# Performance work log

Hardware: AMD Instinct MI355X
Metric: run time of the kernel (lower is better)

The kernel has to match this reference:

```python
import jax, jax.numpy as jnp
import numpy as np

B, T, S, D, V, NX = 4, 256, 400, 512, 50000, 50
VEXT = V + NX  # extended vocab


def setup_inputs() -> dict:
    key = jax.random.key(0)
    ks = jax.random.split(key, 10)
    s = 0.02
    return {
        "x": jax.random.normal(ks[0], (B, T, D), dtype=jnp.float32),
        "enc_outputs": jax.random.normal(ks[1], (B, S, D), dtype=jnp.float32),
        "src_mask": jax.random.randint(ks[2], (B, 1, S), 0, 2, dtype=jnp.int32),
        "enc_batch_extend_vocab": jax.random.randint(ks[3], (B, S), 0, VEXT, dtype=jnp.int64),
        "extra_zeros": jnp.zeros((B, T, NX), dtype=jnp.float32),
        "fc_w": jax.random.normal(ks[4], (V, D), dtype=jnp.float32) * s,
        "fc_b": jnp.zeros((V,), dtype=jnp.float32),
        "pgen_w": jax.random.normal(ks[5], (1, D), dtype=jnp.float32) * s,
        "pgen_b": jnp.zeros((1,), dtype=jnp.float32),
        "wq": jax.random.normal(ks[6], (D, D), dtype=jnp.float32) * s,
        "bq": jnp.zeros((D,), dtype=jnp.float32),
        "wk": jax.random.normal(ks[7], (D, D), dtype=jnp.float32) * s,
        "bk": jnp.zeros((D,), dtype=jnp.float32),
    }


def reference(x, enc_outputs, src_mask, enc_batch_extend_vocab, extra_zeros,
              fc_w, fc_b, pgen_w, pgen_b, wq, bq, wk, bk):
    # vocab distribution: [B,T,V]
    p_vocab = jax.nn.softmax(x @ fc_w.T + fc_b, axis=-1)
    # single-head cross attention probs (h=1 -> d_k = D)
    q = x @ wq.T + bq                 # [B,T,D]
    k = enc_outputs @ wk.T + bk       # [B,S,D]
    scores = jnp.einsum('btd,bsd->bts', q, k) / jnp.sqrt(jnp.float32(D))
    scores = jnp.where(src_mask == 0, jnp.float32(-1e9), scores)  # mask [B,1,S]
    attn_probs = jax.nn.softmax(scores, axis=-1)  # [B,T,S]
    # generation gate
    p_gen = jax.nn.sigmoid(x @ pgen_w.T + pgen_b)  # [B,T,1]
    attn_dist = (1.0 - p_gen) * attn_probs         # copy distribution over source
    p_ext = jnp.concatenate([p_gen * p_vocab, extra_zeros], axis=-1)  # [B,T,VEXT]
    # scatter-add copy probs into extended vocab slots
    b_idx = jnp.arange(B)[:, None, None]
    t_idx = jnp.arange(T)[None, :, None]
    v_idx = enc_batch_extend_vocab[:, None, :]
    bb, tt, vv = jnp.broadcast_arrays(b_idx, t_idx, v_idx)  # each [B,T,S]
    p_ext = p_ext.at[bb, tt, vv].add(attn_dist)
    return jnp.log(jnp.maximum(p_ext, jnp.float32(1e-9)))
```

## Files before the change

### kernel.cpp

```cpp
#include <hip/hip_runtime.h>
#include <hip/hip_bf16.h>
#include <math.h>

constexpr int cB = 4, cT = 256, cS = 400, cD = 512, cV = 50000, cNX = 50;
constexpr int cVEXT = cV + cNX;
constexpr int cPAN  = (cV + 127) / 128;
constexpr int cCBLD = cVEXT * 2;
constexpr int cTOP  = 50100;
constexpr int cMQ   = cB * cT;

typedef __attribute__((ext_vector_type(8))) short short8v;
typedef __attribute__((ext_vector_type(4))) float floatx4;

__device__ inline ushort f2bf(float f) {
    union { float f; unsigned u; } v; v.f = f;
    unsigned r = (v.u + 0x7FFFu + ((v.u >> 16) & 1u)) >> 16;
    return (ushort)r;
}
__device__ inline float bf2f(ushort u) {
    union { unsigned u; float f; } v; v.u = ((unsigned)u) << 16;
    return v.f;
}

__global__ __launch_bounds__(256) void cast_kernel(
    const float* __restrict__ src, ushort* __restrict__ dst, int n4)
{
    const int stride = gridDim.x * 256;
    for (int i = blockIdx.x * 256 + threadIdx.x; i < n4; i += stride) {
        float4 v = *(const float4*)(src + (size_t)i * 4);
        ushort4 o;
        o.x = f2bf(v.x); o.y = f2bf(v.y); o.z = f2bf(v.z); o.w = f2bf(v.w);
        *(ushort4*)(dst + (size_t)i * 4) = o;
    }
}

__global__ __launch_bounds__(256) void gemm_proj(
    const ushort* __restrict__ A, const ushort* __restrict__ Wb,
    const float* __restrict__ bias, float* __restrict__ Cf,
    int M, int N, int K, int ldc)
{
    __shared__ ushort As[2][128 * 32];
    __shared__ ushort Bs[2][128 * 32];

    const int tid  = threadIdx.x;
    const int lane = tid & 63;
    const int wv   = tid >> 6;
    const int wm   = wv >> 1;
    const int wn   = wv & 1;
    const int bm   = blockIdx.x * 128;
    const int bn   = blockIdx.y * 128;

    const int rA = lane & 15;
    const int kA = (lane >> 4) * 8;
    const int nt = K >> 5;

    floatx4 acc[4][4] = {};

    auto stage = [&](int bidx, int t) {
        const int k0 = t * 32;
        #pragma unroll
        for (int c = 0; c < 2; ++c) {
            const int chunk = wv * 2 + c;
            int ga = bm + chunk * 16 + rA; if (ga >= M) ga = M - 1;
            __builtin_amdgcn_global_load_lds(
                (const __attribute__((address_space(1))) void*)(A + (size_t)ga * K + k0 + kA),
                (__attribute__((address_space(3))) void*)&As[bidx][chunk * 512], 16, 0, 0);
            int gb = bn + chunk * 16 + rA; if (gb >= N) gb = N - 1;
            __builtin_amdgcn_global_load_lds(
                (const __attribute__((address_space(1))) void*)(Wb + (size_t)gb * K + k0 + kA),
                (__attribute__((address_space(3))) void*)&Bs[bidx][chunk * 512], 16, 0, 0);
        }
    };

    stage(0, 0);
    __syncthreads();

    int buf = 0;
    for (int t = 0; t < nt; ++t) {
        if (t + 1 < nt) stage(buf ^ 1, t + 1);
        short8v a[4], b[4];
        #pragma unroll
        for (int mi = 0; mi < 4; ++mi)
            a[mi] = *(const short8v*)&As[buf][(wm * 4 + mi) * 512 + lane * 8];
        #pragma unroll
        for (int ni = 0; ni < 4; ++ni)
            b[ni] = *(const short8v*)&Bs[buf][(wn * 4 + ni) * 512 + lane * 8];
        #pragma unroll
        for (int mi = 0; mi < 4; ++mi)
            #pragma unroll
            for (int ni = 0; ni < 4; ++ni)
                acc[mi][ni] = __builtin_amdgcn_mfma_f32_16x16x32_bf16(
                    a[mi], b[ni], acc[mi][ni], 0, 0, 0);
        __syncthreads();
        buf ^= 1;
    }

    const int fr = lane & 15;
    const int g  = lane >> 4;
    #pragma unroll
    for (int mi = 0; mi < 4; ++mi) {
        #pragma unroll
        for (int ni = 0; ni < 4; ++ni) {
            const int colg = bn + wn * 64 + ni * 16 + fr;
            if (colg >= N) continue;
            const float bv = bias[colg];
            #pragma unroll
            for (int r = 0; r < 4; ++r) {
                const int row = bm + wm * 64 + mi * 16 + g * 4 + r;
                if (row < M) Cf[(size_t)row * ldc + colg] = acc[mi][ni][r] + bv;
            }
        }
    }
}

__global__ __launch_bounds__(256) void gemm_big(
    const ushort* __restrict__ A, const ushort* __restrict__ Wb,
    const float* __restrict__ bias, ushort* __restrict__ Cb,
    float* __restrict__ pm, float* __restrict__ ps)
{
    __shared__ ushort As[2][128 * 32];
    __shared__ ushort Bs[2][128 * 32];
    __shared__ float sm_m[2][128];
    __shared__ float sm_s[2][128];

    const int tid  = threadIdx.x;
    const int lane = tid & 63;
    const int wv   = tid >> 6;
    const int wm   = wv >> 1;
    const int wn   = wv & 1;

    const int wg  = blockIdx.y * gridDim.x + blockIdx.x;
    const int nwg = gridDim.x * gridDim.y;
    const int j   = (wg & 7) * (nwg >> 3) + (wg >> 3);
    const int pan = j >> 3;
    const int bm  = (j & 7) * 128;
    const int bn  = pan * 128;

    const int srow = lane >> 2;
    const int sk   = (lane & 3) * 8;

    floatx4 acc[4][4] = {};

    auto stage = [&](int bidx, int t) {
        const int k0 = t * 32;
        #pragma unroll
        for (int c = 0; c < 2; ++c) {
            const int lr = wv * 32 + c * 16;
            const int ga = bm + lr + srow;
            __builtin_amdgcn_global_load_lds(
                (const __attribute__((address_space(1))) void*)(A + (size_t)ga * cD + k0 + sk),
                (__attribute__((address_space(3))) void*)&As[bidx][lr * 32], 16, 0, 0);
        }
        #pragma unroll
        for (int c = 0; c < 2; ++c) {
            const int lr = wv * 32 + c * 16;
            int gb = bn + lr + srow; if (gb >= cV) gb = cV - 1;
            __builtin_amdgcn_global_load_lds(
                (const __attribute__((address_space(1))) void*)(Wb + (size_t)gb * cD + k0 + sk),
                (__attribute__((address_space(3))) void*)&Bs[bidx][lr * 32], 16, 0, 0);
        }
    };

    stage(0, 0);
    __syncthreads();

    const int fr = lane & 15;
    const int g  = lane >> 4;
    int buf = 0;

    #pragma unroll 1
    for (int t = 0; t < 16; ++t) {
        if (t + 1 < 16) stage(buf ^ 1, t + 1);
        short8v a[4], b[4];
        #pragma unroll
        for (int mi = 0; mi < 4; ++mi)
            a[mi] = *(const short8v*)&As[buf][(wm * 64 + mi * 16 + fr) * 32 + g * 8];
        #pragma unroll
        for (int ni = 0; ni < 4; ++ni)
            b[ni] = *(const short8v*)&Bs[buf][(wn * 64 + ni * 16 + fr) * 32 + g * 8];
        #pragma unroll
        for (int mi = 0; mi < 4; ++mi)
            #pragma unroll
            for (int ni = 0; ni < 4; ++ni)
                acc[mi][ni] = __builtin_amdgcn_mfma_f32_16x16x32_bf16(
                    a[mi], b[ni], acc[mi][ni], 0, 0, 0);
        __syncthreads();
        buf ^= 1;
    }

    float bv[4]; bool val[4];
    #pragma unroll
    for (int ni = 0; ni < 4; ++ni) {
        const int colg = bn + wn * 64 + ni * 16 + fr;
        val[ni] = (colg < cV);
        bv[ni] = val[ni] ? bias[colg] : 0.f;
    }
    #pragma unroll
    for (int mi = 0; mi < 4; ++mi)
        #pragma unroll
        for (int ni = 0; ni < 4; ++ni)
            #pragma unroll
            for (int r = 0; r < 4; ++r)
                acc[mi][ni][r] += bv[ni];

    #pragma unroll
    for (int mi = 0; mi < 4; ++mi) {
        #pragma unroll
        for (int r = 0; r < 4; ++r) {
            float mx = -1e30f;
            #pragma unroll
            for (int ni = 0; ni < 4; ++ni)
                if (val[ni]) mx = fmaxf(mx, acc[mi][ni][r]);
            #pragma unroll
            for (int sw = 1; sw < 16; sw <<= 1)
                mx = fmaxf(mx, __shfl_xor(mx, sw));
            float sm = 0.f;
            #pragma unroll
            for (int ni = 0; ni < 4; ++ni)
                if (val[ni]) sm += __expf(acc[mi][ni][r] - mx);
            #pragma unroll
            for (int sw = 1; sw < 16; sw <<= 1)
                sm += __shfl_xor(sm, sw);
            if (fr == 0) {
                const int rl = wm * 64 + mi * 16 + g * 4 + r;
                sm_m[wn][rl] = mx;
                sm_s[wn][rl] = sm;
            }
        }
    }
    __syncthreads();
    if (tid < 128) {
        const float m0 = sm_m[0][tid], m1 = sm_m[1][tid];
        const float s0 = sm_s[0][tid], s1 = sm_s[1][tid];
        const float mm = fmaxf(m0, m1);
        const float ss = s0 * __expf(m0 - mm) + s1 * __expf(m1 - mm);
        const int grow = bm + tid;
        pm[(size_t)pan * cMQ + grow] = mm;
        ps[(size_t)pan * cMQ + grow] = ss;
    }

    #pragma unroll
    for (int mi = 0; mi < 4; ++mi) {
        #pragma unroll
        for (int ni = 0; ni < 4; ++ni) {
            if (!val[ni]) continue;
            const int colg = bn + wn * 64 + ni * 16 + fr;
            #pragma unroll
            for (int r = 0; r < 4; ++r) {
                const int row = bm + wm * 64 + mi * 16 + g * 4 + r;
                Cb[(size_t)row * cCBLD + cTOP + colg] = f2bf(acc[mi][ni][r]);
            }
        }
    }
}

__global__ __launch_bounds__(256) void combine_kernel(
    const float* __restrict__ pm, const float* __restrict__ ps,
    const float* __restrict__ pgen, float* __restrict__ rowadd)
{
    const int lane = threadIdx.x & 63;
    const int wv   = threadIdx.x >> 6;
    const int row  = blockIdx.x * 64 + lane;

    float m = -1e30f, s = 0.f;
    #pragma unroll 2
    for (int i = wv; i < cPAN; i += 4) {
        const float mi = pm[(size_t)i * cMQ + row];
        const float si = ps[(size_t)i * cMQ + row];
        const float nm = fmaxf(m, mi);
        s = s * __expf(m - nm) + si * __expf(mi - nm);
        m = nm;
    }
    __shared__ float rm[4][64], rs[4][64];
    rm[wv][lane] = m; rs[wv][lane] = s;
    __syncthreads();
    if (wv == 0) {
        m = rm[0][lane]; s = rs[0][lane];
        #pragma unroll
        for (int i = 1; i < 4; ++i) {
            const float m2 = rm[i][lane], s2 = rs[i][lane];
            const float nm = fmaxf(m, m2);
            s = s * __expf(m - nm) + s2 * __expf(m2 - nm);
            m = nm;
        }
        rowadd[row] = __logf(pgen[row]) - m - __logf(s);
    }
}

__global__ __launch_bounds__(512) void transform_reg(
    float* __restrict__ out, const float* __restrict__ rowadd,
    const int* __restrict__ ebev, const float* __restrict__ attn)
{
    const int row = blockIdx.x;
    const int b   = row / cT;
    const int tid = threadIdx.x;
    constexpr float LOGMIN = -20.72326583694641f;
    constexpr int NCHUNK = cV / 8;

    __shared__ int   pos[cS];
    __shared__ float add[cS];
    for (int s = tid; s < cS; s += 512) {
        pos[s] = ebev[b * cS + s];
        add[s] = attn[(size_t)row * cS + s];
    }

    const float a = rowadd[row];
    const ushort* rowu = (const ushort*)out + (size_t)row * cCBLD + cTOP;
    float* rowf = out + (size_t)row * cVEXT;

    constexpr int BLO[5] = {0, 4, 7, 10, 13};
    #pragma unroll
    for (int bb = 0; bb < 4; ++bb) {
        ushort4 lo[4], hi[4];
        #pragma unroll
        for (int s = 0; s < 4; ++s) {
            const int t = BLO[bb] + s;
            if (t < BLO[bb + 1]) {
                const int cidx = t * 512 + tid;
                if (cidx < NCHUNK) {
                    lo[s] = *(const ushort4*)(rowu + (size_t)cidx * 8);
                    hi[s] = *(const ushort4*)(rowu + (size_t)cidx * 8 + 4);
                }
            }
        }
        __syncthreads();
        #pragma unroll
        for (int s = 0; s < 4; ++s) {
            const int t = BLO[bb] + s;
            if (t < BLO[bb + 1]) {
                const int cidx = t * 512 + tid;
                if (cidx < NCHUNK) {
                    const int jb = cidx * 8;
                    float2 o;
                    o.x = fmaxf(bf2f(lo[s].x) + a, LOGMIN);
                    o.y = fmaxf(bf2f(lo[s].y) + a, LOGMIN);
                    *(float2*)(rowf + jb) = o;
                    o.x = fmaxf(bf2f(lo[s].z) + a, LOGMIN);
                    o.y = fmaxf(bf2f(lo[s].w) + a, LOGMIN);
                    *(float2*)(rowf + jb + 2) = o;
                    o.x = fmaxf(bf2f(hi[s].x) + a, LOGMIN);
                    o.y = fmaxf(bf2f(hi[s].y) + a, LOGMIN);
                    *(float2*)(rowf + jb + 4) = o;
                    o.x = fmaxf(bf2f(hi[s].z) + a, LOGMIN);
                    o.y = fmaxf(bf2f(hi[s].w) + a, LOGMIN);
                    *(float2*)(rowf + jb + 6) = o;
                }
            }
        }
    }
    if (tid < (cVEXT - cV) / 2) {
        float2 z; z.x = LOGMIN; z.y = LOGMIN;
        *(float2*)(rowf + cV + 2 * tid) = z;
    }
    __syncthreads();

    for (int s = tid; s < cS; s += 512) {
        const int p = pos[s];
        bool leader = true;
        for (int s2 = 0; s2 < s; ++s2)
            if (pos[s2] == p) { leader = false; break; }
        if (!leader) continue;
        float sum = add[s];
        for (int s2 = s + 1; s2 < cS; ++s2)
            if (pos[s2] == p) sum += add[s2];
        const float base = __expf(rowf[p]);
        rowf[p] = __logf(fmaxf(base + sum, 1e-9f));
    }
}

__global__ __launch_bounds__(64) void pgen_kernel(
    const float* __restrict__ x, const float* __restrict__ w,
    const float* __restrict__ b, float* __restrict__ pgen)
{
    const int row = blockIdx.x;
    const int lane = threadIdx.x;
    const float* xr = x + (size_t)row * cD;
    float s = 0.f;
    for (int i = lane; i < cD; i += 64) s += xr[i] * w[i];
    #pragma unroll
    for (int off = 32; off; off >>= 1) s += __shfl_down(s, off);
    if (lane == 0) pgen[row] = 1.f / (1.f + __expf(-(s + b[0])));
}

__global__ __launch_bounds__(256) void attn_kernel(
    const float* __restrict__ q, const float* __restrict__ k,
    const int* __restrict__ src_mask, const float* __restrict__ pgen,
    float* __restrict__ attn)
{
    constexpr float scale = 0.04419417382415922f;
    const int row = blockIdx.x;
    const int b = row / cT;
    const int tid = threadIdx.x;

    __shared__ __align__(16) float qs[cD];
    __shared__ float sc[cS];
    __shared__ float red[4];

    for (int i = tid; i < cD; i += 256) qs[i] = q[(size_t)row * cD + i];
    __syncthreads();

    for (int s = tid; s < cS; s += 256) {
        const float* kr = k + ((size_t)b * cS + s) * cD;
        float dot = 0.f;
        #pragma unroll 4
        for (int i = 0; i < cD; i += 4) {
            float4 kv = *(const float4*)(kr + i);
            float4 qv = *(const float4*)(qs + i);
            dot += qv.x * kv.x + qv.y * kv.y + qv.z * kv.z + qv.w * kv.w;
        }
        float v = dot * scale;
        if (src_mask[b * cS + s] == 0) v = -1e9f;
        sc[s] = v;
    }
    __syncthreads();

    float m = -3.4e38f;
    for (int s = tid; s < cS; s += 256) m = fmaxf(m, sc[s]);
    #pragma unroll
    for (int off = 32; off; off >>= 1) m = fmaxf(m, __shfl_down(m, off));
    if ((tid & 63) == 0) red[tid >> 6] = m;
    __syncthreads();
    m = fmaxf(fmaxf(red[0], red[1]), fmaxf(red[2], red[3]));
    __syncthreads();

    float sum = 0.f;
    for (int s = tid; s < cS; s += 256) {
        float e = __expf(sc[s] - m);
        sc[s] = e;
        sum += e;
    }
    #pragma unroll
    for (int off = 32; off; off >>= 1) sum += __shfl_down(sum, off);
    if ((tid & 63) == 0) red[tid >> 6] = sum;
    __syncthreads();
    sum = red[0] + red[1] + red[2] + red[3];

    const float w = (1.f - pgen[row]) / sum;
    for (int s = tid; s < cS; s += 256)
        attn[(size_t)row * cS + s] = sc[s] * w;
}

extern "C" void kernel_launch(void* const* d_in, const int* in_sizes, int n_in,
                              void* d_out, int out_size, void* d_ws, size_t ws_size,
                              hipStream_t stream)
{
    const float* x      = (const float*)d_in[0];
    const float* enc    = (const float*)d_in[1];
    const int*   mask   = (const int*)d_in[2];
    const int*   ebev   = (const int*)d_in[3];
    const float* fc_w   = (const float*)d_in[5];
    const float* fc_b   = (const float*)d_in[6];
    const float* pgen_w = (const float*)d_in[7];
    const float* pgen_b = (const float*)d_in[8];
    const float* wq     = (const float*)d_in[9];
    const float* bq     = (const float*)d_in[10];
    const float* wk     = (const float*)d_in[11];
    const float* bk     = (const float*)d_in[12];
    float* out = (float*)d_out;

    float* ws     = (float*)d_ws;
    float* q      = ws;
    float* kbuf   = q + (size_t)cB * cT * cD;
    float* pgen   = kbuf + (size_t)cB * cS * cD;
    float* attn   = pgen + cB * cT;
    float* pm     = attn + (size_t)cB * cT * cS;
    float* ps     = pm + (size_t)cPAN * cMQ;
    float* rowadd = ps + (size_t)cPAN * cMQ;
    ushort* xb    = (ushort*)(rowadd + cMQ);
    ushort* encb  = xb + (size_t)cB * cT * cD;
    ushort* wqb   = encb + (size_t)cB * cS * cD;
    ushort* wkb   = wqb + (size_t)cD * cD;
    ushort* wb    = wkb + (size_t)cD * cD;

    const dim3 blk(256);
    const int MQ = cMQ;
    const int MK = cB * cS;

    cast_kernel<<<dim3(512), blk, 0, stream>>>(x, xb, (cB * cT * cD) / 4);
    cast_kernel<<<dim3(512), blk, 0, stream>>>(enc, encb, (cB * cS * cD) / 4);
    cast_kernel<<<dim3(256), blk, 0, stream>>>(wq, wqb, (cD * cD) / 4);
    cast_kernel<<<dim3(256), blk, 0, stream>>>(wk, wkb, (cD * cD) / 4);
    cast_kernel<<<dim3(2048), blk, 0, stream>>>(fc_w, wb, (cV * cD) / 4);

    gemm_proj<<<dim3(MQ / 128, cD / 128), blk, 0, stream>>>(
        xb, wqb, bq, q, MQ, cD, cD, cD);
    gemm_proj<<<dim3((MK + 127) / 128, cD / 128), blk, 0, stream>>>(
        encb, wkb, bk, kbuf, MK, cD, cD, cD);
    pgen_kernel<<<dim3(MQ), dim3(64), 0, stream>>>(x, pgen_w, pgen_b, pgen);

    attn_kernel<<<dim3(MQ), blk, 0, stream>>>(q, kbuf, mask, pgen, attn);

    gemm_big<<<dim3(8, cPAN), blk, 0, stream>>>(
        xb, wb, fc_b, (ushort*)out, pm, ps);

    combine_kernel<<<dim3(MQ / 64), blk, 0, stream>>>(pm, ps, pgen, rowadd);

    transform_reg<<<dim3(MQ), dim3(512), 0, stream>>>(out, rowadd, ebev, attn);
}
```

Baseline: 414.8 us.

## Double M tile of vocab GEMM, fuse pgen into attention, merge small casts

```diff
diff --git a/kernel.cpp b/kernel.cpp
--- a/kernel.cpp
+++ b/kernel.cpp
@@ -31,6 +31,29 @@
         ushort4 o;
         o.x = f2bf(v.x); o.y = f2bf(v.y); o.z = f2bf(v.z); o.w = f2bf(v.w);
         *(ushort4*)(dst + (size_t)i * 4) = o;
+    }
+}
+
+__global__ __launch_bounds__(256) void cast4_kernel(
+    const float* __restrict__ s0, ushort* __restrict__ d0, int n0,
+    const float* __restrict__ s1, ushort* __restrict__ d1, int n1,
+    const float* __restrict__ s2, ushort* __restrict__ d2, int n2,
+    const float* __restrict__ s3, ushort* __restrict__ d3, int n3)
+{
+    const int stride = gridDim.x * 256;
+    const int base = blockIdx.x * 256 + threadIdx.x;
+    const float* ss[4] = {s0, s1, s2, s3};
+    ushort*      dd[4] = {d0, d1, d2, d3};
+    const int    nn[4] = {n0, n1, n2, n3};
+    #pragma unroll
+    for (int seg = 0; seg < 4; ++seg) {
+        const float* s = ss[seg]; ushort* d = dd[seg]; const int n = nn[seg];
+        for (int i = base; i < n; i += stride) {
+            float4 v = *(const float4*)(s + (size_t)i * 4);
+            ushort4 o;
+            o.x = f2bf(v.x); o.y = f2bf(v.y); o.z = f2bf(v.z); o.w = f2bf(v.w);
+            *(ushort4*)(d + (size_t)i * 4) = o;
+        }
     }
 }
 
@@ -118,10 +141,10 @@
     const float* __restrict__ bias, ushort* __restrict__ Cb,
     float* __restrict__ pm, float* __restrict__ ps)
 {
-    __shared__ ushort As[2][128 * 32];
+    __shared__ ushort As[2][2][128 * 32];
     __shared__ ushort Bs[2][128 * 32];
-    __shared__ float sm_m[2][128];
-    __shared__ float sm_s[2][128];
+    __shared__ float sm_m[2][256];
+    __shared__ float sm_s[2][256];
 
     const int tid  = threadIdx.x;
     const int lane = tid & 63;
@@ -131,26 +154,31 @@
 
     const int wg  = blockIdx.y * gridDim.x + blockIdx.x;
     const int nwg = gridDim.x * gridDim.y;
-    const int j   = (wg & 7) * (nwg >> 3) + (wg >> 3);
-    const int pan = j >> 3;
-    const int bm  = (j & 7) * 128;
+    const int qq  = nwg >> 3, rr = nwg & 7;
+    const int xcd = wg & 7;
+    const int j   = (xcd < rr ? xcd * (qq + 1) : rr * (qq + 1) + (xcd - rr) * qq)
+                  + (wg >> 3);
+    const int pan = j >> 2;
+    const int bm  = (j & 3) * 256;
     const int bn  = pan * 128;
 
     const int srow = lane >> 2;
     const int sk   = (lane & 3) * 8;
 
-    floatx4 acc[4][4] = {};
+    floatx4 acc[2][4][4] = {};
 
     auto stage = [&](int bidx, int t) {
         const int k0 = t * 32;
         #pragma unroll
-        for (int c = 0; c < 2; ++c) {
-            const int lr = wv * 32 + c * 16;
-            const int ga = bm + lr + srow;
-            __builtin_amdgcn_global_load_lds(
-                (const __attribute__((address_space(1))) void*)(A + (size_t)ga * cD + k0 + sk),
-                (__attribute__((address_space(3))) void*)&As[bidx][lr * 32], 16, 0, 0);
-        }
+        for (int h = 0; h < 2; ++h)
+            #pragma unroll
+            for (int c = 0; c < 2; ++c) {
+                const int lr = wv * 32 + c * 16;
+                const int ga = bm + h * 128 + lr + srow;
+                __builtin_amdgcn_global_load_lds(
+                    (const __attribute__((address_space(1))) void*)(A + (size_t)ga * cD + k0 + sk),
+                    (__attribute__((address_space(3))) void*)&As[h][bidx][lr * 32], 16, 0, 0);
+            }
         #pragma unroll
         for (int c = 0; c < 2; ++c) {
             const int lr = wv * 32 + c * 16;
@@ -171,19 +199,23 @@
     #pragma unroll 1
     for (int t = 0; t < 16; ++t) {
         if (t + 1 < 16) stage(buf ^ 1, t + 1);
-        short8v a[4], b[4];
-        #pragma unroll
-        for (int mi = 0; mi < 4; ++mi)
-            a[mi] = *(const short8v*)&As[buf][(wm * 64 + mi * 16 + fr) * 32 + g * 8];
+        short8v a[2][4], b[4];
+        #pragma unroll
+        for (int h = 0; h < 2; ++h)
+            #pragma unroll
+            for (int mi = 0; mi < 4; ++mi)
+                a[h][mi] = *(const short8v*)&As[h][buf][(wm * 64 + mi * 16 + fr) * 32 + g * 8];
         #pragma unroll
         for (int ni = 0; ni < 4; ++ni)
             b[ni] = *(const short8v*)&Bs[buf][(wn * 64 + ni * 16 + fr) * 32 + g * 8];
         #pragma unroll
-        for (int mi = 0; mi < 4; ++mi)
-            #pragma unroll
-            for (int ni = 0; ni < 4; ++ni)
-                acc[mi][ni] = __builtin_amdgcn_mfma_f32_16x16x32_bf16(
-                    a[mi], b[ni], acc[mi][ni], 0, 0, 0);
+        for (int h = 0; h < 2; ++h)
+            #pragma unroll
+            for (int mi = 0; mi < 4; ++mi)
+                #pragma unroll
+                for (int ni = 0; ni < 4; ++ni)
+                    acc[h][mi][ni] = __builtin_amdgcn_mfma_f32_16x16x32_bf16(
+                        a[h][mi], b[ni], acc[h][mi][ni], 0, 0, 0);
         __syncthreads();
         buf ^= 1;
     }
@@ -196,40 +228,45 @@
         bv[ni] = val[ni] ? bias[colg] : 0.f;
     }
     #pragma unroll
-    for (int mi = 0; mi < 4; ++mi)
-        #pragma unroll
-        for (int ni = 0; ni < 4; ++ni)
-            #pragma unroll
-            for (int r = 0; r < 4; ++r)
-                acc[mi][ni][r] += bv[ni];
-
-    #pragma unroll
-    for (int mi = 0; mi < 4; ++mi) {
-        #pragma unroll
-        for (int r = 0; r < 4; ++r) {
-            float mx = -1e30f;
+    for (int h = 0; h < 2; ++h)
+        #pragma unroll
+        for (int mi = 0; mi < 4; ++mi)
             #pragma unroll
             for (int ni = 0; ni < 4; ++ni)
-                if (val[ni]) mx = fmaxf(mx, acc[mi][ni][r]);
-            #pragma unroll
-            for (int sw = 1; sw < 16; sw <<= 1)
-                mx = fmaxf(mx, __shfl_xor(mx, sw));
-            float sm = 0.f;
-            #pragma unroll
-            for (int ni = 0; ni < 4; ++ni)
-                if (val[ni]) sm += __expf(acc[mi][ni][r] - mx);
-            #pragma unroll
-            for (int sw = 1; sw < 16; sw <<= 1)
-                sm += __shfl_xor(sm, sw);
-            if (fr == 0) {
-                const int rl = wm * 64 + mi * 16 + g * 4 + r;
-                sm_m[wn][rl] = mx;
-                sm_s[wn][rl] = sm;
+                #pragma unroll
+                for (int r = 0; r < 4; ++r)
+                    acc[h][mi][ni][r] += bv[ni];
+
+    #pragma unroll
+    for (int h = 0; h < 2; ++h) {
+        #pragma unroll
+        for (int mi = 0; mi < 4; ++mi) {
+            #pragma unroll
+            for (int r = 0; r < 4; ++r) {
+                float mx = -1e30f;
+                #pragma unroll
+                for (int ni = 0; ni < 4; ++ni)
+                    if (val[ni]) mx = fmaxf(mx, acc[h][mi][ni][r]);
+                #pragma unroll
+                for (int sw = 1; sw < 16; sw <<= 1)
+                    mx = fmaxf(mx, __shfl_xor(mx, sw));
+                float sm = 0.f;
+                #pragma unroll
+                for (int ni = 0; ni < 4; ++ni)
+                    if (val[ni]) sm += __expf(acc[h][mi][ni][r] - mx);
+                #pragma unroll
+                for (int sw = 1; sw < 16; sw <<= 1)
+                    sm += __shfl_xor(sm, sw);
+                if (fr == 0) {
+                    const int rl = h * 128 + wm * 64 + mi * 16 + g * 4 + r;
+                    sm_m[wn][rl] = mx;
+                    sm_s[wn][rl] = sm;
+                }
             }
         }
     }
     __syncthreads();
-    if (tid < 128) {
+    {
         const float m0 = sm_m[0][tid], m1 = sm_m[1][tid];
         const float s0 = sm_s[0][tid], s1 = sm_s[1][tid];
         const float mm = fmaxf(m0, m1);
@@ -240,15 +277,18 @@
     }
 
     #pragma unroll
-    for (int mi = 0; mi < 4; ++mi) {
-        #pragma unroll
-        for (int ni = 0; ni < 4; ++ni) {
-            if (!val[ni]) continue;
-            const int colg = bn + wn * 64 + ni * 16 + fr;
-            #pragma unroll
-            for (int r = 0; r < 4; ++r) {
-                const int row = bm + wm * 64 + mi * 16 + g * 4 + r;
-                Cb[(size_t)row * cCBLD + cTOP + colg] = f2bf(acc[mi][ni][r]);
+    for (int h = 0; h < 2; ++h) {
+        #pragma unroll
+        for (int mi = 0; mi < 4; ++mi) {
+            #pragma unroll
+            for (int ni = 0; ni < 4; ++ni) {
+                if (!val[ni]) continue;
+                const int colg = bn + wn * 64 + ni * 16 + fr;
+                #pragma unroll
+                for (int r = 0; r < 4; ++r) {
+                    const int row = bm + h * 128 + wm * 64 + mi * 16 + g * 4 + r;
+                    Cb[(size_t)row * cCBLD + cTOP + colg] = f2bf(acc[h][mi][ni][r]);
+                }
             }
         }
     }
@@ -368,24 +408,12 @@
     }
 }
 
-__global__ __launch_bounds__(64) void pgen_kernel(
-    const float* __restrict__ x, const float* __restrict__ w,
-    const float* __restrict__ b, float* __restrict__ pgen)
-{
-    const int row = blockIdx.x;
-    const int lane = threadIdx.x;
-    const float* xr = x + (size_t)row * cD;
-    float s = 0.f;
-    for (int i = lane; i < cD; i += 64) s += xr[i] * w[i];
-    #pragma unroll
-    for (int off = 32; off; off >>= 1) s += __shfl_down(s, off);
-    if (lane == 0) pgen[row] = 1.f / (1.f + __expf(-(s + b[0])));
-}
-
 __global__ __launch_bounds__(256) void attn_kernel(
     const float* __restrict__ q, const float* __restrict__ k,
-    const int* __restrict__ src_mask, const float* __restrict__ pgen,
-    float* __restrict__ attn)
+    const int* __restrict__ src_mask,
+    const float* __restrict__ x, const float* __restrict__ pgw,
+    const float* __restrict__ pgb,
+    float* __restrict__ pgen, float* __restrict__ attn)
 {
     constexpr float scale = 0.04419417382415922f;
     const int row = blockIdx.x;
@@ -395,8 +423,23 @@
     __shared__ __align__(16) float qs[cD];
     __shared__ float sc[cS];
     __shared__ float red[4];
-
-    for (int i = tid; i < cD; i += 256) qs[i] = q[(size_t)row * cD + i];
+    __shared__ float spg;
+
+    float pg = 0.f;
+    for (int i = tid; i < cD; i += 256) {
+        qs[i] = q[(size_t)row * cD + i];
+        pg += x[(size_t)row * cD + i] * pgw[i];
+    }
+    #pragma unroll
+    for (int off = 32; off; off >>= 1) pg += __shfl_down(pg, off);
+    if ((tid & 63) == 0) red[tid >> 6] = pg;
+    __syncthreads();
+    if (tid == 0) {
+        const float d = red[0] + red[1] + red[2] + red[3];
+        const float pv = 1.f / (1.f + __expf(-(d + pgb[0])));
+        pgen[row] = pv;
+        spg = pv;
+    }
     __syncthreads();
 
     for (int s = tid; s < cS; s += 256) {
@@ -435,7 +478,7 @@
     __syncthreads();
     sum = red[0] + red[1] + red[2] + red[3];
 
-    const float w = (1.f - pgen[row]) / sum;
+    const float w = (1.f - spg) / sum;
     for (int s = tid; s < cS; s += 256)
         attn[(size_t)row * cS + s] = sc[s] * w;
 }
@@ -476,21 +519,22 @@
     const int MQ = cMQ;
     const int MK = cB * cS;
 
-    cast_kernel<<<dim3(512), blk, 0, stream>>>(x, xb, (cB * cT * cD) / 4);
-    cast_kernel<<<dim3(512), blk, 0, stream>>>(enc, encb, (cB * cS * cD) / 4);
-    cast_kernel<<<dim3(256), blk, 0, stream>>>(wq, wqb, (cD * cD) / 4);
-    cast_kernel<<<dim3(256), blk, 0, stream>>>(wk, wkb, (cD * cD) / 4);
+    cast4_kernel<<<dim3(768), blk, 0, stream>>>(
+        x, xb, (cB * cT * cD) / 4,
+        enc, encb, (cB * cS * cD) / 4,
+        wq, wqb, (cD * cD) / 4,
+        wk, wkb, (cD * cD) / 4);
     cast_kernel<<<dim3(2048), blk, 0, stream>>>(fc_w, wb, (cV * cD) / 4);
 
     gemm_proj<<<dim3(MQ / 128, cD / 128), blk, 0, stream>>>(
         xb, wqb, bq, q, MQ, cD, cD, cD);
     gemm_proj<<<dim3((MK + 127) / 128, cD / 128), blk, 0, stream>>>(
         encb, wkb, bk, kbuf, MK, cD, cD, cD);
-    pgen_kernel<<<dim3(MQ), dim3(64), 0, stream>>>(x, pgen_w, pgen_b, pgen);
-
-    attn_kernel<<<dim3(MQ), blk, 0, stream>>>(q, kbuf, mask, pgen, attn);
-
-    gemm_big<<<dim3(8, cPAN), blk, 0, stream>>>(
+
+    attn_kernel<<<dim3(MQ), blk, 0, stream>>>(
+        q, kbuf, mask, x, pgen_w, pgen_b, pgen, attn);
+
+    gemm_big<<<dim3(4, cPAN), blk, 0, stream>>>(
         xb, wb, fc_b, (ushort*)out, pm, ps);
 
     combine_kernel<<<dim3(MQ / 64), blk, 0, stream>>>(pm, ps, pgen, rowadd);
```

Measured after the change: 503.2 us. 1.21x slower.
